# Performance work log

Measured on AMD Instinct MI355X. Metric: run time of the kernel, lower is better.

## Reference

```python
import jax, jax.numpy as jnp
import numpy as np

N_NODES = 100000
N_EDGES = 1600000  # total after symmetrization (800k pairs + reverses)
N_GRAPHS = 64
D_IN = 64
D_HID = 128
N_CLASSES = 10


def setup_inputs() -> dict:
    key = jax.random.key(0)
    ks = jax.random.split(key, 16)
    half = N_EDGES // 2
    src = jax.random.randint(ks[0], (half,), 0, N_NODES)
    dst = jax.random.randint(ks[1], (half,), 0, N_NODES)
    dst = jnp.where(dst == src, (dst + 1) % N_NODES, dst)  # no self-loops
    # to_undirected: symmetric edge list with fixed shape [2, E]
    edge_index = jnp.stack([jnp.concatenate([src, dst]),
                            jnp.concatenate([dst, src])]).astype(jnp.int64)
    # sorted balanced graph assignment: every graph id present
    batch = ((jnp.arange(N_NODES) * N_GRAPHS) // N_NODES).astype(jnp.int64)

    def lin(k, fi, fo):
        return jax.random.normal(k, (fi, fo), jnp.float32) * (1.0 / np.sqrt(fi))

    inp = {
        'x': jax.random.normal(ks[2], (N_NODES, D_IN), jnp.float32),
        'edge_index': edge_index,
        'batch': batch,
        'gin1_w1': lin(ks[3], D_IN, D_HID), 'gin1_b1': jnp.zeros((D_HID,), jnp.float32),
        'gin1_w2': lin(ks[4], D_HID, D_HID), 'gin1_b2': jnp.zeros((D_HID,), jnp.float32),
        'gin2_w1': lin(ks[5], D_HID, D_HID), 'gin2_b1': jnp.zeros((D_HID,), jnp.float32),
        'gin2_w2': lin(ks[6], D_HID, D_HID), 'gin2_b2': jnp.zeros((D_HID,), jnp.float32),
        'gin3_w1': lin(ks[7], D_HID, D_HID), 'gin3_b1': jnp.zeros((D_HID,), jnp.float32),
        'gin3_w2': lin(ks[8], D_HID, D_HID), 'gin3_b2': jnp.zeros((D_HID,), jnp.float32),
        'fc1_w': lin(ks[9], D_HID, 64), 'fc1_b': jnp.zeros((64,), jnp.float32),
        'fc2_w': lin(ks[10], 64, N_CLASSES), 'fc2_b': jnp.zeros((N_CLASSES,), jnp.float32),
    }
    return inp


def _gin_layer(x, src, dst, w1, b1, w2, b2):
    # GINConv (eps=0): h_i = MLP(x_i + sum_{j in N(i)} x_j)
    agg = jax.ops.segment_sum(x[src], dst, num_segments=N_NODES)
    h = x + agg
    h = jax.nn.relu(h @ w1 + b1)
    return h @ w2 + b2


def reference(x, edge_index, batch,
              gin1_w1, gin1_b1, gin1_w2, gin1_b2,
              gin2_w1, gin2_b1, gin2_w2, gin2_b2,
              gin3_w1, gin3_b1, gin3_w2, gin3_b2,
              fc1_w, fc1_b, fc2_w, fc2_b):
    src, dst = edge_index[0], edge_index[1]
    h = _gin_layer(x, src, dst, gin1_w1, gin1_b1, gin1_w2, gin1_b2)
    h = _gin_layer(h, src, dst, gin2_w1, gin2_b1, gin2_w2, gin2_b2)
    h = _gin_layer(h, src, dst, gin3_w1, gin3_b1, gin3_w2, gin3_b2)
    # global_max_pool over graphs
    pooled = jax.ops.segment_max(h, batch, num_segments=N_GRAPHS)  # [G, D_HID]
    out = jax.nn.relu(pooled @ fc1_w + fc1_b) @ fc2_w + fc2_b
    return jax.nn.log_softmax(out, axis=1)
```

## Files before the change

kernel.cpp:

```cpp
#include <hip/hip_runtime.h>
#include <hip/hip_bf16.h>
#include <cmath>

#define NNODES 100000
#define NGRAPHS 64
#define SHIFT 10
#define NPB 1024
#define NB 98
#define CAP 24576
#define BIN_CHUNK 4096
#define HSTRIDE 136
#define CONVBLK 6250

typedef __attribute__((ext_vector_type(8))) short bf16x8;
typedef __attribute__((ext_vector_type(4))) float f32x4;
typedef __attribute__((ext_vector_type(4))) unsigned int u32x4;

__device__ __forceinline__ float bf2f(unsigned short u) {
    unsigned int v = ((unsigned int)u) << 16;
    return __uint_as_float(v);
}
__device__ __forceinline__ unsigned short f2bf(float f) {
    unsigned int v = __float_as_uint(f);
    unsigned int r = (v + 0x7fffu + ((v >> 16) & 1u)) >> 16;
    return (unsigned short)r;
}

__device__ __forceinline__ void atomicMaxF(float* addr, float v) {
    if (v >= 0.f) atomicMax((int*)addr, __float_as_int(v));
    else          atomicMin((unsigned int*)addr, __float_as_uint(v));
}

__device__ __forceinline__ void pack_one(unsigned short* wp, const float* W, int K, int t) {
    int total = (K / 32) * 8 * 64;
    if (t >= total) return;
    int l = t & 63;
    int n0 = (t >> 6) & 7;
    int kp = t >> 9;
    unsigned short o[8];
#pragma unroll
    for (int j = 0; j < 8; ++j)
        o[j] = f2bf(W[(size_t)(kp * 32 + (l >> 4) * 8 + j) * 128 + n0 * 16 + (l & 15)]);
    *(u32x4*)(wp + (size_t)t * 8) = *(u32x4*)o;
}

__global__ __launch_bounds__(256) void setup_kernel(
        unsigned short* __restrict__ B0, const float* __restrict__ x,
        unsigned short* wp1, const float* g1w1,
        unsigned short* wp2, const float* g1w2,
        unsigned short* wp3, const float* g2w1,
        unsigned short* wp4, const float* g2w2,
        unsigned short* wp5, const float* g3w1,
        unsigned short* wp6, const float* g3w2,
        float* __restrict__ pooled, int* __restrict__ gcur) {
    int b = blockIdx.x;
    int t = threadIdx.x;
    if (b < CONVBLK) {
        int i = b * 256 + t;
        float4 v = ((const float4*)x)[i];
        unsigned short o[4] = { f2bf(v.x), f2bf(v.y), f2bf(v.z), f2bf(v.w) };
        ((uint2*)B0)[i] = *(uint2*)o;
        return;
    }
    b -= CONVBLK;
    if (b < 44) {
        if (b < 4)       pack_one(wp1, g1w1, 64,  b * 256 + t);
        else if (b < 12) pack_one(wp2, g1w2, 128, (b - 4) * 256 + t);
        else if (b < 20) pack_one(wp3, g2w1, 128, (b - 12) * 256 + t);
        else if (b < 28) pack_one(wp4, g2w2, 128, (b - 20) * 256 + t);
        else if (b < 36) pack_one(wp5, g3w1, 128, (b - 28) * 256 + t);
        else             pack_one(wp6, g3w2, 128, (b - 36) * 256 + t);
        return;
    }
    b -= 44;
    if (b < 32) {
        pooled[b * 256 + t] = -INFINITY;
        return;
    }
    if (t < NB) gcur[t] = t * CAP;
}

__global__ __launch_bounds__(256) void bin_kernel(unsigned int* __restrict__ binned,
                                                  int* __restrict__ gcur,
                                                  const int* __restrict__ ei, int E) {
    __shared__ int cnt[NB];
    __shared__ int gbase[NB];
    __shared__ int loff[NB];
    int t = threadIdx.x;
    int base = blockIdx.x * BIN_CHUNK;
    for (int i = t; i < NB; i += 256) { cnt[i] = 0; loff[i] = 0; }
    __syncthreads();
    unsigned int pk[16]; short bk[16]; int ne = 0;
#pragma unroll
    for (int i = 0; i < 16; ++i) {
        int e = base + t + i * 256;
        if (e < E) {
            int s = ei[e], d = ei[E + e];
            int b = d >> SHIFT;
            pk[ne] = ((unsigned int)s << SHIFT) | (unsigned int)(d & (NPB - 1));
            bk[ne] = (short)b;
            ne++;
            atomicAdd(&cnt[b], 1);
        }
    }
    __syncthreads();
    for (int i = t; i < NB; i += 256)
        gbase[i] = cnt[i] ? atomicAdd(&gcur[i], cnt[i]) : 0;
    __syncthreads();
    for (int i = 0; i < ne; ++i) {
        int b = bk[i];
        int pos = atomicAdd(&loff[b], 1);
        binned[gbase[b] + pos] = pk[i];
    }
}

__global__ __launch_bounds__(256) void fill2_kernel(int* __restrict__ csr,
                                                    int* __restrict__ start,
                                                    const unsigned int* __restrict__ binned,
                                                    const int* __restrict__ gcur, int N) {
    __shared__ int cur[NPB];
    __shared__ int tsum[256];
    __shared__ int gbs[2];
    int b = blockIdx.x, t = threadIdx.x;
    int n0 = b << SHIFT;
    int nn = N - n0; if (nn > NPB) nn = NPB;
    int c = gcur[b] - b * CAP;
    if (t == 0) {
        int acc = 0, tot = 0;
        for (int i = 0; i < NB; ++i) {
            int ci = gcur[i] - i * CAP;
            if (i < b) acc += ci;
            tot += ci;
        }
        gbs[0] = acc; gbs[1] = tot;
    }
    const unsigned int* eb = binned + (size_t)b * CAP;
    for (int i = t; i < NPB; i += 256) cur[i] = 0;
    __syncthreads();
    int gb = gbs[0];
    for (int p = t; p < c; p += 256) atomicAdd(&cur[eb[p] & (NPB - 1)], 1);
    __syncthreads();
    int v[4]; int s = 0;
#pragma unroll
    for (int i = 0; i < 4; ++i) { v[i] = cur[t * 4 + i]; s += v[i]; }
    int x = s;
    tsum[t] = x;
    __syncthreads();
    for (int off = 1; off < 256; off <<= 1) {
        int y = (t >= off) ? tsum[t - off] : 0;
        __syncthreads();
        x += y;
        tsum[t] = x;
        __syncthreads();
    }
    int run = x - s + gb;
#pragma unroll
    for (int i = 0; i < 4; ++i) {
        int idx = t * 4 + i;
        cur[idx] = run;
        if (idx < nn) start[n0 + idx] = run;
        run += v[i];
    }
    __syncthreads();
    for (int p = t; p < c; p += 256) {
        unsigned int e = eb[p];
        int slot = atomicAdd(&cur[e & (NPB - 1)], 1);
        csr[slot] = (int)(e >> SHIFT);
    }
    if (t == 0 && b == 0) start[N] = gbs[1];
}

template<int LANES>
__global__ __launch_bounds__(256) void gather_kernel(unsigned short* __restrict__ outb,
                                                     const unsigned short* __restrict__ h,
                                                     const int* __restrict__ start,
                                                     const int* __restrict__ csr, int N) {
    const int D = LANES * 8;
    int t = threadIdx.x;
    int node = blockIdx.x * (256 / LANES) + t / LANES;
    if (node >= N) return;
    int lane = t % LANES;
    const unsigned short* hb = h + lane * 8;

    float a0[8], a1[8];
    {
        u32x4 v = *(const u32x4*)(hb + (size_t)node * D);
        const unsigned short* q = (const unsigned short*)&v;
#pragma unroll
        for (int i = 0; i < 8; ++i) { a0[i] = bf2f(q[i]); a1[i] = 0.f; }
    }
    int p0 = start[node], p1 = start[node + 1];
    int p = p0;
    for (; p + 4 <= p1; p += 4) {
        int j0 = csr[p], j1 = csr[p + 1], j2 = csr[p + 2], j3 = csr[p + 3];
        u32x4 v0 = *(const u32x4*)(hb + (size_t)j0 * D);
        u32x4 v1 = *(const u32x4*)(hb + (size_t)j1 * D);
        u32x4 v2 = *(const u32x4*)(hb + (size_t)j2 * D);
        u32x4 v3 = *(const u32x4*)(hb + (size_t)j3 * D);
        const unsigned short* q0 = (const unsigned short*)&v0;
        const unsigned short* q1 = (const unsigned short*)&v1;
        const unsigned short* q2 = (const unsigned short*)&v2;
        const unsigned short* q3 = (const unsigned short*)&v3;
#pragma unroll
        for (int i = 0; i < 8; ++i) a0[i] += bf2f(q0[i]);
#pragma unroll
        for (int i = 0; i < 8; ++i) a1[i] += bf2f(q1[i]);
#pragma unroll
        for (int i = 0; i < 8; ++i) a0[i] += bf2f(q2[i]);
#pragma unroll
        for (int i = 0; i < 8; ++i) a1[i] += bf2f(q3[i]);
    }
    for (; p < p1; ++p) {
        int j = csr[p];
        u32x4 v = *(const u32x4*)(hb + (size_t)j * D);
        const unsigned short* q = (const unsigned short*)&v;
#pragma unroll
        for (int i = 0; i < 8; ++i) a0[i] += bf2f(q[i]);
    }
    unsigned short o[8];
#pragma unroll
    for (int i = 0; i < 8; ++i) o[i] = f2bf(a0[i] + a1[i]);
    *(u32x4*)(outb + (size_t)node * D + lane * 8) = *(u32x4*)o;
}

template<int K1, bool POOL>
__global__ __launch_bounds__(256) void mfma_gemm_pair(const unsigned short* __restrict__ A,
                                                      const unsigned short* __restrict__ Wp1,
                                                      const float* __restrict__ bias1,
                                                      const unsigned short* __restrict__ Wp2,
                                                      const float* __restrict__ bias2,
                                                      unsigned short* __restrict__ out,
                                                      const int* __restrict__ batch,
                                                      float* __restrict__ pooled, int M) {
    __shared__ unsigned short hl[4][16 * HSTRIDE];
    __shared__ unsigned int lmax[2][128];
    const int l = threadIdx.x & 63;
    const int w = threadIdx.x >> 6;
    const int mbase = (blockIdx.x * 4 + w) * 16;
    const int kgrp = l >> 4;
    const int col = l & 15;
    int row_a = mbase + col;
    if (row_a >= M) row_a = M - 1;

    if (POOL) {
        for (int i = threadIdx.x; i < 256; i += 256)
            ((unsigned int*)lmax)[i] = 0x007fffffu;
    }

    f32x4 acc[8];
#pragma unroll
    for (int i = 0; i < 8; ++i) acc[i] = (f32x4){0.f, 0.f, 0.f, 0.f};
#pragma unroll
    for (int kp = 0; kp < K1 / 32; ++kp) {
        bf16x8 a = *(const bf16x8*)(A + (size_t)row_a * K1 + kp * 32 + kgrp * 8);
#pragma unroll
        for (int n0 = 0; n0 < 8; ++n0) {
            bf16x8 bfr = *(const bf16x8*)(Wp1 + ((size_t)(kp * 8 + n0) * 64 + l) * 8);
            acc[n0] = __builtin_amdgcn_mfma_f32_16x16x32_bf16(a, bfr, acc[n0], 0, 0, 0);
        }
    }

    unsigned short* hb = hl[w];
#pragma unroll
    for (int n0 = 0; n0 < 8; ++n0) {
        float bv = bias1[n0 * 16 + col];
#pragma unroll
        for (int r = 0; r < 4; ++r) {
            float v = acc[n0][r] + bv;
            v = fmaxf(v, 0.f);
            hb[(kgrp * 4 + r) * HSTRIDE + n0 * 16 + col] = f2bf(v);
        }
    }
    __syncthreads();

    f32x4 acc2[8];
#pragma unroll
    for (int i = 0; i < 8; ++i) acc2[i] = (f32x4){0.f, 0.f, 0.f, 0.f};
#pragma unroll
    for (int kp = 0; kp < 4; ++kp) {
        bf16x8 a2 = *(const bf16x8*)(hb + col * HSTRIDE + kp * 32 + kgrp * 8);
#pragma unroll
        for (int n0 = 0; n0 < 8; ++n0) {
            bf16x8 bfr = *(const bf16x8*)(Wp2 + ((size_t)(kp * 8 + n0) * 64 + l) * 8);
            acc2[n0] = __builtin_amdgcn_mfma_f32_16x16x32_bf16(a2, bfr, acc2[n0], 0, 0, 0);
        }
    }

    if (POOL) {
        int g0 = batch[blockIdx.x * 64];
        int gi[4]; bool ok[4];
#pragma unroll
        for (int r = 0; r < 4; ++r) {
            int row = mbase + kgrp * 4 + r;
            ok[r] = (row < M);
            gi[r] = ok[r] ? (batch[row] - g0) : 0;
        }
#pragma unroll
        for (int n0 = 0; n0 < 8; ++n0) {
            int f = n0 * 16 + col;
            float bv = bias2[f];
#pragma unroll
            for (int r = 0; r < 4; ++r) {
                if (ok[r]) {
                    float v = acc2[n0][r] + bv;
                    unsigned int u = __float_as_uint(v);
                    unsigned int key = (u & 0x80000000u) ? ~u : (u | 0x80000000u);
                    atomicMax(&lmax[gi[r]][f], key);
                }
            }
        }
        __syncthreads();
        int t = threadIdx.x;
        unsigned int key = ((unsigned int*)lmax)[t];
        unsigned int u2 = (key & 0x80000000u) ? (key & 0x7fffffffu) : ~key;
        float v = __uint_as_float(u2);
        int g = g0 + (t >> 7);
        if (g < NGRAPHS && key != 0x007fffffu)
            atomicMaxF(&pooled[g * 128 + (t & 127)], v);
    } else {
#pragma unroll
        for (int n0 = 0; n0 < 8; ++n0) {
            float bv = bias2[n0 * 16 + col];
#pragma unroll
            for (int r = 0; r < 4; ++r) {
                int row = mbase + kgrp * 4 + r;
                if (row < M)
                    out[(size_t)row * 128 + n0 * 16 + col] = f2bf(acc2[n0][r] + bv);
            }
        }
    }
}

__global__ __launch_bounds__(64) void head_kernel(float* __restrict__ out,
                                                  const float* __restrict__ pooled,
                                                  const float* __restrict__ w1,
                                                  const float* __restrict__ b1,
                                                  const float* __restrict__ w2,
                                                  const float* __restrict__ b2) {
    int g = blockIdx.x, t = threadIdx.x;
    __shared__ float a[64];
    __shared__ float o[10];
    __shared__ float red[2];
    const float* pg = pooled + g * 128;
    float acc = b1[t];
    for (int k = 0; k < 128; ++k) acc = fmaf(pg[k], w1[k * 64 + t], acc);
    a[t] = fmaxf(acc, 0.f);
    __syncthreads();
    if (t < 10) {
        float s = b2[t];
        for (int k = 0; k < 64; ++k) s = fmaf(a[k], w2[k * 10 + t], s);
        o[t] = s;
    }
    __syncthreads();
    if (t == 0) {
        float m = -INFINITY;
        for (int c = 0; c < 10; ++c) m = fmaxf(m, o[c]);
        float se = 0.f;
        for (int c = 0; c < 10; ++c) se += expf(o[c] - m);
        red[0] = m;
        red[1] = logf(se);
    }
    __syncthreads();
    if (t < 10) out[g * 10 + t] = o[t] - red[0] - red[1];
}

extern "C" void kernel_launch(void* const* d_in, const int* in_sizes, int n_in,
                              void* d_out, int out_size, void* d_ws, size_t ws_size,
                              hipStream_t stream) {
    const float* x    = (const float*)d_in[0];
    const int* ei     = (const int*)d_in[1];
    const int* batch  = (const int*)d_in[2];
    const float* g1w1 = (const float*)d_in[3];  const float* g1b1 = (const float*)d_in[4];
    const float* g1w2 = (const float*)d_in[5];  const float* g1b2 = (const float*)d_in[6];
    const float* g2w1 = (const float*)d_in[7];  const float* g2b1 = (const float*)d_in[8];
    const float* g2w2 = (const float*)d_in[9];  const float* g2b2 = (const float*)d_in[10];
    const float* g3w1 = (const float*)d_in[11]; const float* g3b1 = (const float*)d_in[12];
    const float* g3w2 = (const float*)d_in[13]; const float* g3b2 = (const float*)d_in[14];
    const float* f1w  = (const float*)d_in[15]; const float* f1b  = (const float*)d_in[16];
    const float* f2w  = (const float*)d_in[17]; const float* f2b  = (const float*)d_in[18];
    float* out = (float*)d_out;

    const int N = NNODES;
    const int E = in_sizes[1] / 2;

    char* base = (char*)d_ws;
    auto alloc = [&](size_t bytes) { char* p = base; base += (bytes + 255) & ~(size_t)255; return p; };

    unsigned short* B1 = (unsigned short*)alloc((size_t)N * 128 * 2);
    unsigned short* B2 = (unsigned short*)alloc((size_t)N * 128 * 2);
    unsigned short* B0 = (unsigned short*)alloc((size_t)N * 64 * 2);
    char* shared_region = alloc((size_t)N * 64 * 2);
    unsigned short* B3 = (unsigned short*)shared_region;
    unsigned int* binned = (unsigned int*)shared_region;
    int* csr      = (int*)alloc((size_t)E * 4);
    int* start    = (int*)alloc((size_t)(N + 1) * 4);
    int* gcur     = (int*)alloc((size_t)(NB + 4) * 4);
    float* pooled = (float*)alloc((size_t)NGRAPHS * 128 * 4);
    unsigned short* wp1 = (unsigned short*)alloc((size_t)64 * 128 * 2);
    unsigned short* wp2 = (unsigned short*)alloc((size_t)128 * 128 * 2);
    unsigned short* wp3 = (unsigned short*)alloc((size_t)128 * 128 * 2);
    unsigned short* wp4 = (unsigned short*)alloc((size_t)128 * 128 * 2);
    unsigned short* wp5 = (unsigned short*)alloc((size_t)128 * 128 * 2);
    unsigned short* wp6 = (unsigned short*)alloc((size_t)128 * 128 * 2);

    setup_kernel<<<CONVBLK + 44 + 32 + 1, 256, 0, stream>>>(
        B0, x, wp1, g1w1, wp2, g1w2, wp3, g2w1, wp4, g2w2, wp5, g3w1, wp6, g3w2,
        pooled, gcur);
    bin_kernel<<<(E + BIN_CHUNK - 1) / BIN_CHUNK, 256, 0, stream>>>(binned, gcur, ei, E);
    fill2_kernel<<<NB, 256, 0, stream>>>(csr, start, binned, gcur, N);

    const int pgrid = (N + 63) / 64;

    gather_kernel<8><<<(N + 31) / 32, 256, 0, stream>>>(B3, B0, start, csr, N);
    mfma_gemm_pair<64, false><<<pgrid, 256, 0, stream>>>(B3, wp1, g1b1, wp2, g1b2, B1, batch, pooled, N);

    gather_kernel<16><<<(N + 15) / 16, 256, 0, stream>>>(B2, B1, start, csr, N);
    mfma_gemm_pair<128, false><<<pgrid, 256, 0, stream>>>(B2, wp3, g2b1, wp4, g2b2, B1, batch, pooled, N);

    gather_kernel<16><<<(N + 15) / 16, 256, 0, stream>>>(B2, B1, start, csr, N);
    mfma_gemm_pair<128, true><<<pgrid, 256, 0, stream>>>(B2, wp5, g3b1, wp6, g3b2, B1, batch, pooled, N);

    head_kernel<<<NGRAPHS, 64, 0, stream>>>(out, pooled, f1w, f1b, f2w, f2b);
}
```

Measured before the change: 303.1 us.

## Fuse neighbor gather into the per-layer MFMA MLP kernel

```diff
diff --git a/kernel.cpp b/kernel.cpp
--- a/kernel.cpp
+++ b/kernel.cpp
@@ -170,89 +170,88 @@
     if (t == 0 && b == 0) start[N] = gbs[1];
 }
 
-template<int LANES>
-__global__ __launch_bounds__(256) void gather_kernel(unsigned short* __restrict__ outb,
-                                                     const unsigned short* __restrict__ h,
-                                                     const int* __restrict__ start,
-                                                     const int* __restrict__ csr, int N) {
-    const int D = LANES * 8;
-    int t = threadIdx.x;
-    int node = blockIdx.x * (256 / LANES) + t / LANES;
-    if (node >= N) return;
-    int lane = t % LANES;
-    const unsigned short* hb = h + lane * 8;
-
-    float a0[8], a1[8];
-    {
-        u32x4 v = *(const u32x4*)(hb + (size_t)node * D);
-        const unsigned short* q = (const unsigned short*)&v;
-#pragma unroll
-        for (int i = 0; i < 8; ++i) { a0[i] = bf2f(q[i]); a1[i] = 0.f; }
-    }
-    int p0 = start[node], p1 = start[node + 1];
-    int p = p0;
-    for (; p + 4 <= p1; p += 4) {
-        int j0 = csr[p], j1 = csr[p + 1], j2 = csr[p + 2], j3 = csr[p + 3];
-        u32x4 v0 = *(const u32x4*)(hb + (size_t)j0 * D);
-        u32x4 v1 = *(const u32x4*)(hb + (size_t)j1 * D);
-        u32x4 v2 = *(const u32x4*)(hb + (size_t)j2 * D);
-        u32x4 v3 = *(const u32x4*)(hb + (size_t)j3 * D);
-        const unsigned short* q0 = (const unsigned short*)&v0;
-        const unsigned short* q1 = (const unsigned short*)&v1;
-        const unsigned short* q2 = (const unsigned short*)&v2;
-        const unsigned short* q3 = (const unsigned short*)&v3;
-#pragma unroll
-        for (int i = 0; i < 8; ++i) a0[i] += bf2f(q0[i]);
-#pragma unroll
-        for (int i = 0; i < 8; ++i) a1[i] += bf2f(q1[i]);
-#pragma unroll
-        for (int i = 0; i < 8; ++i) a0[i] += bf2f(q2[i]);
-#pragma unroll
-        for (int i = 0; i < 8; ++i) a1[i] += bf2f(q3[i]);
-    }
-    for (; p < p1; ++p) {
-        int j = csr[p];
-        u32x4 v = *(const u32x4*)(hb + (size_t)j * D);
-        const unsigned short* q = (const unsigned short*)&v;
-#pragma unroll
-        for (int i = 0; i < 8; ++i) a0[i] += bf2f(q[i]);
-    }
-    unsigned short o[8];
-#pragma unroll
-    for (int i = 0; i < 8; ++i) o[i] = f2bf(a0[i] + a1[i]);
-    *(u32x4*)(outb + (size_t)node * D + lane * 8) = *(u32x4*)o;
-}
-
 template<int K1, bool POOL>
-__global__ __launch_bounds__(256) void mfma_gemm_pair(const unsigned short* __restrict__ A,
-                                                      const unsigned short* __restrict__ Wp1,
-                                                      const float* __restrict__ bias1,
-                                                      const unsigned short* __restrict__ Wp2,
-                                                      const float* __restrict__ bias2,
-                                                      unsigned short* __restrict__ out,
-                                                      const int* __restrict__ batch,
-                                                      float* __restrict__ pooled, int M) {
-    __shared__ unsigned short hl[4][16 * HSTRIDE];
+__global__ __launch_bounds__(256) void fused_layer(const unsigned short* __restrict__ Hin,
+                                                   const int* __restrict__ start,
+                                                   const int* __restrict__ csr,
+                                                   const unsigned short* __restrict__ Wp1,
+                                                   const float* __restrict__ bias1,
+                                                   const unsigned short* __restrict__ Wp2,
+                                                   const float* __restrict__ bias2,
+                                                   unsigned short* __restrict__ out,
+                                                   const int* __restrict__ batch,
+                                                   float* __restrict__ pooled, int M) {
+    __shared__ unsigned short tile[64 * HSTRIDE];
     __shared__ unsigned int lmax[2][128];
     const int l = threadIdx.x & 63;
     const int w = threadIdx.x >> 6;
-    const int mbase = (blockIdx.x * 4 + w) * 16;
+    const int rbase = blockIdx.x * 64 + w * 16;
+    unsigned short* wt = tile + (w * 16) * HSTRIDE;
+
+    if (POOL) {
+        ((unsigned int*)lmax)[threadIdx.x] = 0x007fffffu;
+        __syncthreads();
+    }
+
+    constexpr int LANES = (K1 == 128) ? 16 : 8;
+    constexpr int RPP = 64 / LANES;
+    const int rg = l / LANES;
+    const int ch = l % LANES;
+    const unsigned short* hbb = Hin + ch * 8;
+#pragma unroll
+    for (int pass = 0; pass < 16 / RPP; ++pass) {
+        int rloc = pass * RPP + rg;
+        int row = rbase + rloc;
+        int rowc = row < M ? row : M - 1;
+        float a0[8], a1[8];
+        {
+            u32x4 v = *(const u32x4*)(hbb + (size_t)rowc * K1);
+            const unsigned short* q = (const unsigned short*)&v;
+#pragma unroll
+            for (int i = 0; i < 8; ++i) { a0[i] = bf2f(q[i]); a1[i] = 0.f; }
+        }
+        int p0 = start[rowc], p1 = start[rowc + 1];
+        int p = p0;
+        for (; p + 4 <= p1; p += 4) {
+            int j0 = csr[p], j1 = csr[p + 1], j2 = csr[p + 2], j3 = csr[p + 3];
+            u32x4 v0 = *(const u32x4*)(hbb + (size_t)j0 * K1);
+            u32x4 v1 = *(const u32x4*)(hbb + (size_t)j1 * K1);
+            u32x4 v2 = *(const u32x4*)(hbb + (size_t)j2 * K1);
+            u32x4 v3 = *(const u32x4*)(hbb + (size_t)j3 * K1);
+            const unsigned short* q0 = (const unsigned short*)&v0;
+            const unsigned short* q1 = (const unsigned short*)&v1;
+            const unsigned short* q2 = (const unsigned short*)&v2;
+            const unsigned short* q3 = (const unsigned short*)&v3;
+#pragma unroll
+            for (int i = 0; i < 8; ++i) a0[i] += bf2f(q0[i]);
+#pragma unroll
+            for (int i = 0; i < 8; ++i) a1[i] += bf2f(q1[i]);
+#pragma unroll
+            for (int i = 0; i < 8; ++i) a0[i] += bf2f(q2[i]);
+#pragma unroll
+            for (int i = 0; i < 8; ++i) a1[i] += bf2f(q3[i]);
+        }
+        for (; p < p1; ++p) {
+            int j = csr[p];
+            u32x4 v = *(const u32x4*)(hbb + (size_t)j * K1);
+            const unsigned short* q = (const unsigned short*)&v;
+#pragma unroll
+            for (int i = 0; i < 8; ++i) a0[i] += bf2f(q[i]);
+        }
+        unsigned short o[8];
+#pragma unroll
+        for (int i = 0; i < 8; ++i) o[i] = f2bf(a0[i] + a1[i]);
+        *(u32x4*)(wt + rloc * HSTRIDE + ch * 8) = *(u32x4*)o;
+    }
+
     const int kgrp = l >> 4;
     const int col = l & 15;
-    int row_a = mbase + col;
-    if (row_a >= M) row_a = M - 1;
-
-    if (POOL) {
-        for (int i = threadIdx.x; i < 256; i += 256)
-            ((unsigned int*)lmax)[i] = 0x007fffffu;
-    }
-
     f32x4 acc[8];
 #pragma unroll
     for (int i = 0; i < 8; ++i) acc[i] = (f32x4){0.f, 0.f, 0.f, 0.f};
 #pragma unroll
     for (int kp = 0; kp < K1 / 32; ++kp) {
-        bf16x8 a = *(const bf16x8*)(A + (size_t)row_a * K1 + kp * 32 + kgrp * 8);
+        bf16x8 a = *(const bf16x8*)(wt + col * HSTRIDE + kp * 32 + kgrp * 8);
 #pragma unroll
         for (int n0 = 0; n0 < 8; ++n0) {
             bf16x8 bfr = *(const bf16x8*)(Wp1 + ((size_t)(kp * 8 + n0) * 64 + l) * 8);
@@ -260,7 +259,6 @@
         }
     }
 
-    unsigned short* hb = hl[w];
 #pragma unroll
     for (int n0 = 0; n0 < 8; ++n0) {
         float bv = bias1[n0 * 16 + col];
@@ -268,17 +266,16 @@
         for (int r = 0; r < 4; ++r) {
             float v = acc[n0][r] + bv;
             v = fmaxf(v, 0.f);
-            hb[(kgrp * 4 + r) * HSTRIDE + n0 * 16 + col] = f2bf(v);
-        }
-    }
-    __syncthreads();
+            wt[(kgrp * 4 + r) * HSTRIDE + n0 * 16 + col] = f2bf(v);
+        }
+    }
 
     f32x4 acc2[8];
 #pragma unroll
     for (int i = 0; i < 8; ++i) acc2[i] = (f32x4){0.f, 0.f, 0.f, 0.f};
 #pragma unroll
     for (int kp = 0; kp < 4; ++kp) {
-        bf16x8 a2 = *(const bf16x8*)(hb + col * HSTRIDE + kp * 32 + kgrp * 8);
+        bf16x8 a2 = *(const bf16x8*)(wt + col * HSTRIDE + kp * 32 + kgrp * 8);
 #pragma unroll
         for (int n0 = 0; n0 < 8; ++n0) {
             bf16x8 bfr = *(const bf16x8*)(Wp2 + ((size_t)(kp * 8 + n0) * 64 + l) * 8);
@@ -286,6 +283,7 @@
         }
     }
 
+    const int mbase = rbase;
     if (POOL) {
         int g0 = batch[blockIdx.x * 64];
         int gi[4]; bool ok[4];
@@ -386,12 +384,11 @@
     char* base = (char*)d_ws;
     auto alloc = [&](size_t bytes) { char* p = base; base += (bytes + 255) & ~(size_t)255; return p; };
 
-    unsigned short* B1 = (unsigned short*)alloc((size_t)N * 128 * 2);
+    char* shared_region = alloc((size_t)N * 128 * 2);
+    unsigned short* B1 = (unsigned short*)shared_region;
+    unsigned int* binned = (unsigned int*)shared_region;
     unsigned short* B2 = (unsigned short*)alloc((size_t)N * 128 * 2);
     unsigned short* B0 = (unsigned short*)alloc((size_t)N * 64 * 2);
-    char* shared_region = alloc((size_t)N * 64 * 2);
-    unsigned short* B3 = (unsigned short*)shared_region;
-    unsigned int* binned = (unsigned int*)shared_region;
     int* csr      = (int*)alloc((size_t)E * 4);
     int* start    = (int*)alloc((size_t)(N + 1) * 4);
     int* gcur     = (int*)alloc((size_t)(NB + 4) * 4);
@@ -411,14 +408,9 @@
 
     const int pgrid = (N + 63) / 64;
 
-    gather_kernel<8><<<(N + 31) / 32, 256, 0, stream>>>(B3, B0, start, csr, N);
-    mfma_gemm_pair<64, false><<<pgrid, 256, 0, stream>>>(B3, wp1, g1b1, wp2, g1b2, B1, batch, pooled, N);
-
-    gather_kernel<16><<<(N + 15) / 16, 256, 0, stream>>>(B2, B1, start, csr, N);
-    mfma_gemm_pair<128, false><<<pgrid, 256, 0, stream>>>(B2, wp3, g2b1, wp4, g2b2, B1, batch, pooled, N);
-
-    gather_kernel<16><<<(N + 15) / 16, 256, 0, stream>>>(B2, B1, start, csr, N);
-    mfma_gemm_pair<128, true><<<pgrid, 256, 0, stream>>>(B2, wp5, g3b1, wp6, g3b2, B1, batch, pooled, N);
+    fused_layer<64, false><<<pgrid, 256, 0, stream>>>(B0, start, csr, wp1, g1b1, wp2, g1b2, B1, batch, pooled, N);
+    fused_layer<128, false><<<pgrid, 256, 0, stream>>>(B1, start, csr, wp3, g2b1, wp4, g2b2, B2, batch, pooled, N);
+    fused_layer<128, true><<<pgrid, 256, 0, stream>>>(B2, start, csr, wp5, g3b1, wp6, g3b2, (unsigned short*)nullptr, batch, pooled, N);
 
     head_kernel<<<NGRAPHS, 64, 0, stream>>>(out, pooled, f1w, f1b, f2w, f2b);
 }
```

Result: no change. 298.7 us (-1.5%).
